# Optimization experiments

Hardware: AMD Instinct MI355X
Metric: run time of the kernel (lower is better)

## Reference

```python
import jax, jax.numpy as jnp
import numpy as np

NUM_HEADS = 4
D_MODEL = 192
NEG_INF = -1000000000.0  # fp32 branch of the original mask fill


def setup_inputs() -> dict:
    key = jax.random.key(0)
    ks = jax.random.split(key, 9)
    b, s, d = 4, 2048, D_MODEL
    inp = {
        "query": jax.random.normal(ks[0], (b, s, d), dtype=jnp.float32),
        "key": jax.random.normal(ks[1], (b, s, d), dtype=jnp.float32),
        "value": jax.random.normal(ks[2], (b, s, d), dtype=jnp.float32),
        "attn_mask": jax.random.randint(ks[3], (b, s, s), 0, 2, dtype=jnp.int32),
        "bias": jax.random.normal(ks[4], (1, NUM_HEADS, s, s), dtype=jnp.float32) * 0.1,
        # nn.Linear(d, d, bias=False) weights, applied as x @ W.T
        "Wq": jax.random.normal(ks[5], (d, d), dtype=jnp.float32) / np.sqrt(d),
        "Wk": jax.random.normal(ks[6], (d, d), dtype=jnp.float32) / np.sqrt(d),
        "Wv": jax.random.normal(ks[7], (d, d), dtype=jnp.float32) / np.sqrt(d),
        "Wo": jax.random.normal(ks[8], (d, d), dtype=jnp.float32) / np.sqrt(d),
    }
    return inp


def reference(query, key, value, attn_mask, bias, Wq, Wk, Wv, Wo):
    b, s, d = query.shape
    h, dh = NUM_HEADS, d // NUM_HEADS
    # QKV projections (Linear, no bias): x @ W.T
    q = (query @ Wq.T).reshape(b, s, h, dh)   # [b,s,h,dh]
    k = (key @ Wk.T).reshape(b, s, h, dh)
    v = (value @ Wv.T).reshape(b, s, h, dh)
    # unscaled dot-product logits (original has no 1/sqrt(d) scaling)
    logits = jnp.einsum("bqhd,bkhd->bhqk", q, k)
    logits = logits + bias                       # bias added BEFORE mask fill
    mask4 = attn_mask[:, None, :, :]             # [b,1,q,k] -> broadcast over heads
    logits = jnp.where(mask4 == 0, NEG_INF, logits)
    weights = jax.nn.softmax(logits, axis=-1)    # [b,h,q,k]
    # dropout_rate=0.0 (eval-mode / identity dropout)
    out = jnp.einsum("bhqk,bkhd->bqhd", weights, v).reshape(b, s, d)
    out = out @ Wo.T
    return out, weights.mean(axis=1)             # ([b,s,d], [b,s,s])
```

## Files before the change

### kernel.cpp

```cpp
#include <hip/hip_runtime.h>

#define BB 4
#define SS 2048
#define HH 4
#define DD 192
#define QT 16
#define NT (SS / 2 / 64)
#define NEG_BIG (-1e9f)
#define MB_NEG 0xCE6Eu

typedef __attribute__((ext_vector_type(8))) short short8;
typedef __attribute__((ext_vector_type(4))) float f32x4;

__device__ inline ushort f2bf(float x) {
    union { float f; unsigned u; } v; v.f = x;
    unsigned r = (v.u + 0x7FFFu + ((v.u >> 16) & 1u)) >> 16;
    return (ushort)r;
}
__device__ inline float bf2f(ushort x) {
    union { unsigned u; float f; } v; v.u = ((unsigned)x) << 16;
    return v.f;
}
__device__ inline void wave_lds_fence() {
    __builtin_amdgcn_wave_barrier();
    __builtin_amdgcn_s_waitcnt(0xC07F);
    __builtin_amdgcn_wave_barrier();
}

__global__ __launch_bounds__(256) void wt_kernel(
    const float* __restrict__ Wq, const float* __restrict__ Wk,
    const float* __restrict__ Wv, const float* __restrict__ Wo,
    float* __restrict__ WTall)
{
    __shared__ float tile[32][33];
    const float* W = (blockIdx.z == 0) ? Wq : (blockIdx.z == 1) ? Wk
                   : (blockIdx.z == 2) ? Wv : Wo;
    float* WT = WTall + (size_t)blockIdx.z * DD * DD;
    const int c0 = blockIdx.x * 32, j0 = blockIdx.y * 32;
    const int tx = threadIdx.x & 31, ty = threadIdx.x >> 5;
#pragma unroll
    for (int k = 0; k < 4; ++k)
        tile[ty + 8 * k][tx] = W[(size_t)(j0 + ty + 8 * k) * DD + c0 + tx];
    __syncthreads();
#pragma unroll
    for (int k = 0; k < 4; ++k)
        WT[(size_t)(c0 + ty + 8 * k) * DD + j0 + tx] = tile[tx][ty + 8 * k];
}

__global__ __launch_bounds__(192) void qkv_proj_kernel(
    const float* __restrict__ Xq, const float* __restrict__ Xk,
    const float* __restrict__ Xv, const float* __restrict__ WTall,
    ushort* __restrict__ qpad, ushort* __restrict__ kpad,
    ushort* __restrict__ vT)
{
    const int mode = blockIdx.y;
    const float* __restrict__ X = (mode == 0) ? Xq : (mode == 1) ? Xk : Xv;
    const float* __restrict__ WT = WTall + (size_t)mode * DD * DD;

    __shared__ __align__(16) float xs[16][DD];
    const int row0 = blockIdx.x * 16;
    const int t = threadIdx.x;
    {
        const float4* src = (const float4*)(X + (size_t)row0 * DD);
        float4* dst = (float4*)&xs[0][0];
        for (int i = t; i < 16 * DD / 4; i += 192) dst[i] = src[i];
    }
    __syncthreads();

    const int jt = (t % 48) * 4;
    const int rowg = t / 48;

    float acc[4][4];
#pragma unroll
    for (int r = 0; r < 4; ++r)
#pragma unroll
        for (int j = 0; j < 4; ++j) acc[r][j] = 0.f;

#pragma unroll 2
    for (int k4 = 0; k4 < DD / 4; ++k4) {
        float4 w0 = *(const float4*)&WT[(size_t)(k4 * 4 + 0) * DD + jt];
        float4 w1 = *(const float4*)&WT[(size_t)(k4 * 4 + 1) * DD + jt];
        float4 w2 = *(const float4*)&WT[(size_t)(k4 * 4 + 2) * DD + jt];
        float4 w3 = *(const float4*)&WT[(size_t)(k4 * 4 + 3) * DD + jt];
#pragma unroll
        for (int r = 0; r < 4; ++r) {
            float4 xv = *(const float4*)&xs[rowg * 4 + r][k4 * 4];
            acc[r][0] = fmaf(xv.x, w0.x, acc[r][0]); acc[r][1] = fmaf(xv.x, w0.y, acc[r][1]);
            acc[r][2] = fmaf(xv.x, w0.z, acc[r][2]); acc[r][3] = fmaf(xv.x, w0.w, acc[r][3]);
            acc[r][0] = fmaf(xv.y, w1.x, acc[r][0]); acc[r][1] = fmaf(xv.y, w1.y, acc[r][1]);
            acc[r][2] = fmaf(xv.y, w1.z, acc[r][2]); acc[r][3] = fmaf(xv.y, w1.w, acc[r][3]);
            acc[r][0] = fmaf(xv.z, w2.x, acc[r][0]); acc[r][1] = fmaf(xv.z, w2.y, acc[r][1]);
            acc[r][2] = fmaf(xv.z, w2.z, acc[r][2]); acc[r][3] = fmaf(xv.z, w2.w, acc[r][3]);
            acc[r][0] = fmaf(xv.w, w3.x, acc[r][0]); acc[r][1] = fmaf(xv.w, w3.y, acc[r][1]);
            acc[r][2] = fmaf(xv.w, w3.z, acc[r][2]); acc[r][3] = fmaf(xv.w, w3.w, acc[r][3]);
        }
    }

    if (mode < 2) {
        ushort* __restrict__ out = (mode == 0) ? qpad : kpad;
        const int hd = jt / 48, f = jt % 48;
#pragma unroll
        for (int r = 0; r < 4; ++r) {
            ushort4 o;
            o.x = f2bf(acc[r][0]); o.y = f2bf(acc[r][1]);
            o.z = f2bf(acc[r][2]); o.w = f2bf(acc[r][3]);
            *(ushort4*)&out[((size_t)(row0 + rowg * 4 + r) * HH + hd) * 64 + f] = o;
        }
        const int4 z = make_int4(0, 0, 0, 0);
        for (int i = t; i < 128; i += 192) {
            const int row = i >> 3, hh = (i >> 1) & 3, half = i & 1;
            *(int4*)&out[((size_t)(row0 + row) * HH + hh) * 64 + 48 + half * 8] = z;
        }
    } else {
        const int b = row0 >> 11, s0 = row0 & (SS - 1);
#pragma unroll
        for (int j = 0; j < 4; ++j) {
            const int col = jt + j, hd = col / 48, f = col % 48;
#pragma unroll
            for (int p = 0; p < 2; ++p) {
                unsigned pk = (unsigned)f2bf(acc[2 * p][j]) |
                              ((unsigned)f2bf(acc[2 * p + 1][j]) << 16);
                *(unsigned*)&vT[(((size_t)b * HH + hd) * 48 + f) * SS +
                                s0 + rowg * 4 + 2 * p] = pk;
            }
        }
    }
}

__device__ inline f32x4 qk_tile(const ushort* kp, short8 qa0, short8 qa1) {
    short8 kb0 = *(const short8*)(kp);
    short8 kb1 = *(const short8*)(kp + 32);
    f32x4 d = {0.f, 0.f, 0.f, 0.f};
    d = __builtin_amdgcn_mfma_f32_16x16x32_bf16(qa0, kb0, d, 0, 0, 0);
    d = __builtin_amdgcn_mfma_f32_16x16x32_bf16(qa1, kb1, d, 0, 0, 0);
    return d;
}

__global__ __launch_bounds__(512, 4) void attn_kernel(
    const ushort* __restrict__ qpad, const ushort* __restrict__ kpad,
    const ushort* __restrict__ vT, const int* __restrict__ mask,
    const float* __restrict__ bias,
    ushort* __restrict__ wscr, float* __restrict__ linv_g,
    float* __restrict__ oattn)
{
    __shared__ __align__(16) ushort wb[2][8][QT][72];
    __shared__ float l_scr[8][QT];

    const int b  = blockIdx.x >> 7;
    const int q0 = (blockIdx.x & 127) * QT;
    const int t = threadIdx.x;
    const int w = t >> 6;
    const int h = w & 3;
    const int kh = w >> 2;
    const int lane = t & 63;
    const int n16 = lane & 15, quad = lane >> 4;
    const int kbase0 = kh * (SS / 2);

    const ushort* qbase =
        qpad + ((size_t)(b * SS + q0 + n16) * HH + h) * 64 + quad * 8;
    const short8 qa0 = *(const short8*)(qbase);
    const short8 qa1 = *(const short8*)(qbase + 32);
    const ushort* kbase = kpad + (size_t)b * SS * HH * 64 + h * 64 + quad * 8;

    const int srow = lane >> 4;
    const int skey = (lane & 15) * 4;
    const int* mrow0 = mask + (size_t)(b * SS + q0) * SS + kbase0 + skey;
    const float* brow0 = bias + (size_t)(h * SS + q0) * SS + kbase0 + skey;

    float l_[4] = {0.f, 0.f, 0.f, 0.f};
    f32x4 pv[3];
#pragma unroll
    for (int nb = 0; nb < 3; ++nb) pv[nb] = (f32x4){0.f, 0.f, 0.f, 0.f};

    int4  mzc[4];
    float4 bvc[4];
#pragma unroll
    for (int rr = 0; rr < 4; ++rr) {
        const int row = rr * 4 + srow;
        mzc[rr] = *(const int4*)(mrow0 + (size_t)row * SS);
        bvc[rr] = *(const float4*)(brow0 + (size_t)row * SS);
    }
#pragma unroll
    for (int rr = 0; rr < 4; ++rr) {
        const int row = rr * 4 + srow;
        ushort4 o;
        o.x = mzc[rr].x ? f2bf(bvc[rr].x) : (ushort)MB_NEG;
        o.y = mzc[rr].y ? f2bf(bvc[rr].y) : (ushort)MB_NEG;
        o.z = mzc[rr].z ? f2bf(bvc[rr].z) : (ushort)MB_NEG;
        o.w = mzc[rr].w ? f2bf(bvc[rr].w) : (ushort)MB_NEG;
        *(ushort4*)&wb[0][w][row][skey] = o;
    }
#pragma unroll
    for (int rr = 0; rr < 4; ++rr) {
        const int row = rr * 4 + srow;
        mzc[rr] = *(const int4*)(mrow0 + (size_t)row * SS + 64);
        bvc[rr] = *(const float4*)(brow0 + (size_t)row * SS + 64);
    }
    wave_lds_fence();

    int buf = 0;
    for (int kt = 0; kt < NT; ++kt) {
        const int kb = kt * 64;

#pragma unroll
        for (int g = 0; g < 4; ++g) {
            const int key = kbase0 + kb + g * 16 + n16;
            f32x4 d = qk_tile(kbase + (size_t)key * (HH * 64), qa0, qa1);
#pragma unroll
            for (int r = 0; r < 4; ++r) {
                float wgt = __expf(d[r] + bf2f(wb[buf][w][quad * 4 + r][g * 16 + n16]));
                l_[r] += wgt;
                wb[buf][w][quad * 4 + r][g * 16 + n16] = f2bf(wgt);
            }
        }

        wave_lds_fence();

        if (kt + 1 < NT) {
#pragma unroll
            for (int rr = 0; rr < 4; ++rr) {
                const int row = rr * 4 + srow;
                ushort4 o;
                o.x = mzc[rr].x ? f2bf(bvc[rr].x) : (ushort)MB_NEG;
                o.y = mzc[rr].y ? f2bf(bvc[rr].y) : (ushort)MB_NEG;
                o.z = mzc[rr].z ? f2bf(bvc[rr].z) : (ushort)MB_NEG;
                o.w = mzc[rr].w ? f2bf(bvc[rr].w) : (ushort)MB_NEG;
                *(ushort4*)&wb[buf ^ 1][w][row][skey] = o;
            }
        }
        if (kt + 2 < NT) {
#pragma unroll
            for (int rr = 0; rr < 4; ++rr) {
                const int row = rr * 4 + srow;
                mzc[rr] = *(const int4*)(mrow0 + (size_t)row * SS + kb + 128);
                bvc[rr] = *(const float4*)(brow0 + (size_t)row * SS + kb + 128);
            }
        }

        const short8 wa0 = *(const short8*)&wb[buf][w][n16][quad * 8];
        const short8 wa1 = *(const short8*)&wb[buf][w][n16][32 + quad * 8];
#pragma unroll
        for (int nb = 0; nb < 3; ++nb) {
            const ushort* vb = vT + ((size_t)(b * HH + h) * 48 + nb * 16 + n16) * SS
                               + kbase0 + kb + quad * 8;
            short8 v0 = *(const short8*)(vb);
            short8 v1 = *(const short8*)(vb + 32);
            pv[nb] = __builtin_amdgcn_mfma_f32_16x16x32_bf16(wa0, v0, pv[nb], 0, 0, 0);
            pv[nb] = __builtin_amdgcn_mfma_f32_16x16x32_bf16(wa1, v1, pv[nb], 0, 0, 0);
        }

        {
            const int r4 = lane >> 4;
            const int k4 = (lane & 15) * 4;
#pragma unroll
            for (int it = 0; it < 4; ++it) {
                const int row = it * 4 + r4;
                ushort4 wv = *(const ushort4*)&wb[buf][w][row][k4];
                *(ushort4*)&wscr[((size_t)(b * SS + q0 + row) * HH + h) * SS +
                                 kbase0 + kb + k4] = wv;
            }
        }

        wave_lds_fence();
        buf ^= 1;
    }

#pragma unroll
    for (int r = 0; r < 4; ++r) {
        float ll = l_[r];
#pragma unroll
        for (int off = 1; off < 16; off <<= 1) ll += __shfl_xor(ll, off);
        l_[r] = ll;
    }
    if (n16 == 0) {
#pragma unroll
        for (int r = 0; r < 4; ++r) l_scr[w][quad * 4 + r] = l_[r];
    }

    __syncthreads();

    float* scr = (float*)&wb[0][0][0][0];
    if (kh == 1) {
#pragma unroll
        for (int nb = 0; nb < 3; ++nb)
            *(f32x4*)&scr[((size_t)(h * 64 + lane)) * 12 + nb * 4] = pv[nb];
    }
    __syncthreads();

    if (kh == 0) {
        float linv[4];
#pragma unroll
        for (int r = 0; r < 4; ++r)
            linv[r] = 1.0f / (l_scr[h][quad * 4 + r] + l_scr[h + 4][quad * 4 + r]);
        if (n16 == 0) {
#pragma unroll
            for (int r = 0; r < 4; ++r)
                linv_g[((size_t)b * HH + h) * SS + q0 + quad * 4 + r] = linv[r];
        }
#pragma unroll
        for (int nb = 0; nb < 3; ++nb) {
            f32x4 po = *(const f32x4*)&scr[((size_t)(h * 64 + lane)) * 12 + nb * 4];
#pragma unroll
            for (int r = 0; r < 4; ++r)
                oattn[((size_t)(b * SS + q0 + quad * 4 + r)) * DD +
                      h * 48 + nb * 16 + n16] = (pv[nb][r] + po[r]) * linv[r];
        }
    }
}

__global__ __launch_bounds__(256) void tail_kernel(
    const float* __restrict__ X,
    const float* __restrict__ WT,
    float* __restrict__ Y,
    const ushort* __restrict__ wscr, const float* __restrict__ linv_g,
    float* __restrict__ out1)
{
    __shared__ __align__(16) float xs[16][DD];
    const int t = threadIdx.x;

    if (blockIdx.x < 512) {
        const int row0 = blockIdx.x * 16;
        {
            const float4* src = (const float4*)(X + (size_t)row0 * DD);
            float4* dst = (float4*)&xs[0][0];
            for (int i = t; i < 16 * DD / 4; i += 256) dst[i] = src[i];
        }
        __syncthreads();
        if (t < 192) {
            const int jt = (t % 48) * 4;
            const int rowg = t / 48;

            float acc[4][4];
#pragma unroll
            for (int r = 0; r < 4; ++r)
#pragma unroll
                for (int j = 0; j < 4; ++j) acc[r][j] = 0.f;

#pragma unroll 2
            for (int k4 = 0; k4 < DD / 4; ++k4) {
                float4 w0 = *(const float4*)&WT[(size_t)(k4 * 4 + 0) * DD + jt];
                float4 w1 = *(const float4*)&WT[(size_t)(k4 * 4 + 1) * DD + jt];
                float4 w2 = *(const float4*)&WT[(size_t)(k4 * 4 + 2) * DD + jt];
                float4 w3 = *(const float4*)&WT[(size_t)(k4 * 4 + 3) * DD + jt];
#pragma unroll
                for (int r = 0; r < 4; ++r) {
                    float4 xv = *(const float4*)&xs[rowg * 4 + r][k4 * 4];
                    acc[r][0] = fmaf(xv.x, w0.x, acc[r][0]); acc[r][1] = fmaf(xv.x, w0.y, acc[r][1]);
                    acc[r][2] = fmaf(xv.x, w0.z, acc[r][2]); acc[r][3] = fmaf(xv.x, w0.w, acc[r][3]);
                    acc[r][0] = fmaf(xv.y, w1.x, acc[r][0]); acc[r][1] = fmaf(xv.y, w1.y, acc[r][1]);
                    acc[r][2] = fmaf(xv.y, w1.z, acc[r][2]); acc[r][3] = fmaf(xv.y, w1.w, acc[r][3]);
                    acc[r][0] = fmaf(xv.z, w2.x, acc[r][0]); acc[r][1] = fmaf(xv.z, w2.y, acc[r][1]);
                    acc[r][2] = fmaf(xv.z, w2.z, acc[r][2]); acc[r][3] = fmaf(xv.z, w2.w, acc[r][3]);
                    acc[r][0] = fmaf(xv.w, w3.x, acc[r][0]); acc[r][1] = fmaf(xv.w, w3.y, acc[r][1]);
                    acc[r][2] = fmaf(xv.w, w3.z, acc[r][2]); acc[r][3] = fmaf(xv.w, w3.w, acc[r][3]);
                }
            }

#pragma unroll
            for (int r = 0; r < 4; ++r)
                *(float4*)&Y[(size_t)(row0 + rowg * 4 + r) * DD + jt] =
                    make_float4(acc[r][0], acc[r][1], acc[r][2], acc[r][3]);
        }
    } else {
        const int bq = blockIdx.x - 512;
        const int b = bq >> 11;
        const int q = bq & (SS - 1);
        const ushort* base = wscr + (size_t)bq * (HH * SS) + t * 8;

        float li[HH];
#pragma unroll
        for (int hh = 0; hh < HH; ++hh)
            li[hh] = linv_g[((size_t)b * HH + hh) * SS + q] * 0.25f;

        float acc[8];
#pragma unroll
        for (int j = 0; j < 8; ++j) acc[j] = 0.f;

#pragma unroll
        for (int hh = 0; hh < HH; ++hh) {
            short8 wv = *(const short8*)(base + (size_t)hh * SS);
#pragma unroll
            for (int j = 0; j < 8; ++j)
                acc[j] = fmaf(bf2f((ushort)wv[j]), li[hh], acc[j]);
        }

        float* dst = out1 + (size_t)bq * SS + t * 8;
        *(float4*)dst = make_float4(acc[0], acc[1], acc[2], acc[3]);
        *(float4*)(dst + 4) = make_float4(acc[4], acc[5], acc[6], acc[7]);
    }
}

extern "C" void kernel_launch(void* const* d_in, const int* in_sizes, int n_in,
                              void* d_out, int out_size, void* d_ws, size_t ws_size,
                              hipStream_t stream)
{
    const float* query = (const float*)d_in[0];
    const float* key   = (const float*)d_in[1];
    const float* value = (const float*)d_in[2];
    const int*   amask = (const int*)d_in[3];
    const float* bias  = (const float*)d_in[4];
    const float* Wq    = (const float*)d_in[5];
    const float* Wk    = (const float*)d_in[6];
    const float* Wv    = (const float*)d_in[7];
    const float* Wo    = (const float*)d_in[8];

    const size_t n_rows = (size_t)BB * SS;
    float* out0 = (float*)d_out;
    float* out1 = out0 + n_rows * DD;

    ushort* qpad  = (ushort*)d_ws;
    ushort* kpad  = qpad + n_rows * HH * 64;
    ushort* vT    = kpad + n_rows * HH * 64;
    float*  oattn = (float*)(vT + (size_t)BB * HH * 48 * SS);
    float*  WTall = oattn + n_rows * DD;
    float*  linvg = WTall + 4 * DD * DD;
    ushort* wscr  = (ushort*)(linvg + (size_t)BB * HH * SS);

    wt_kernel<<<dim3(6, 6, 4), 256, 0, stream>>>(Wq, Wk, Wv, Wo, WTall);

    qkv_proj_kernel<<<dim3(n_rows / 16, 3), 192, 0, stream>>>(
        query, key, value, WTall, qpad, kpad, vT);

    attn_kernel<<<dim3(BB * SS / QT), 512, 0, stream>>>(
        qpad, kpad, vT, amask, bias, wscr, linvg, oattn);

    tail_kernel<<<dim3(512 + BB * SS), 256, 0, stream>>>(
        oattn, WTall + 3 * DD * DD, out0, wscr, linvg, out1);
}
```

Baseline: 378.6 us.

## Store K and V in MFMA-fragment-tiled layout for contiguous per-wave loads

The projection kernel now writes K and V into pre-swizzled 1024-element tiles that match the MFMA B-operand fragment order. Each lane in the attention kernel then reads its short8 at lane*8 within a tile, so a wave's K and V loads become fully contiguous instead of strided across rows of 256 or 2048 elements. In exchange, the projection kernel's stores are more scattered, and the index math must match the fragment mapping exactly.

```diff
diff --git a/kernel.cpp b/kernel.cpp
--- a/kernel.cpp
+++ b/kernel.cpp
@@ -50,8 +50,8 @@
 __global__ __launch_bounds__(192) void qkv_proj_kernel(
     const float* __restrict__ Xq, const float* __restrict__ Xk,
     const float* __restrict__ Xv, const float* __restrict__ WTall,
-    ushort* __restrict__ qpad, ushort* __restrict__ kpad,
-    ushort* __restrict__ vT)
+    ushort* __restrict__ qpad, ushort* __restrict__ kpadT,
+    ushort* __restrict__ vTf)
 {
     const int mode = blockIdx.y;
     const float* __restrict__ X = (mode == 0) ? Xq : (mode == 1) ? Xk : Xv;
@@ -96,49 +96,66 @@
         }
     }
 
-    if (mode < 2) {
-        ushort* __restrict__ out = (mode == 0) ? qpad : kpad;
+    const int b = row0 >> 11, s_base = row0 & (SS - 1);
+
+    if (mode == 0) {
         const int hd = jt / 48, f = jt % 48;
 #pragma unroll
         for (int r = 0; r < 4; ++r) {
             ushort4 o;
             o.x = f2bf(acc[r][0]); o.y = f2bf(acc[r][1]);
             o.z = f2bf(acc[r][2]); o.w = f2bf(acc[r][3]);
-            *(ushort4*)&out[((size_t)(row0 + rowg * 4 + r) * HH + hd) * 64 + f] = o;
+            *(ushort4*)&qpad[((size_t)(row0 + rowg * 4 + r) * HH + hd) * 64 + f] = o;
         }
         const int4 z = make_int4(0, 0, 0, 0);
         for (int i = t; i < 128; i += 192) {
             const int row = i >> 3, hh = (i >> 1) & 3, half = i & 1;
-            *(int4*)&out[((size_t)(row0 + row) * HH + hh) * 64 + 48 + half * 8] = z;
+            *(int4*)&qpad[((size_t)(row0 + row) * HH + hh) * 64 + 48 + half * 8] = z;
+        }
+    } else if (mode == 1) {
+        const int hd = jt / 48, f0 = jt % 48;
+        const int off_base = (f0 < 32)
+            ? ((f0 >> 3) * 16) * 8 + (f0 & 7)
+            : 512 + (((f0 - 32) >> 3) * 16) * 8 + (f0 & 7);
+#pragma unroll
+        for (int r = 0; r < 4; ++r) {
+            const int s = s_base + rowg * 4 + r;
+            ushort4 o;
+            o.x = f2bf(acc[r][0]); o.y = f2bf(acc[r][1]);
+            o.z = f2bf(acc[r][2]); o.w = f2bf(acc[r][3]);
+            const size_t base = ((size_t)(b * HH + hd) * (SS / 16) + (s >> 4)) * 1024;
+            *(ushort4*)&kpadT[base + off_base + (size_t)(s & 15) * 8] = o;
+        }
+        const int4 z = make_int4(0, 0, 0, 0);
+        for (int i = t; i < 128; i += 192) {
+            const int row = i >> 3, hh = (i >> 1) & 3, half = i & 1;
+            const int s = s_base + row;
+            const size_t base = ((size_t)(b * HH + hh) * (SS / 16) + (s >> 4)) * 1024;
+            *(int4*)&kpadT[base + 512 + ((size_t)((2 + half) * 16 + (s & 15))) * 8] = z;
         }
     } else {
-        const int b = row0 >> 11, s0 = row0 & (SS - 1);
 #pragma unroll
         for (int j = 0; j < 4; ++j) {
             const int col = jt + j, hd = col / 48, f = col % 48;
+            const int nb = f >> 4, dfrac = f & 15;
 #pragma unroll
             for (int p = 0; p < 2; ++p) {
+                const int s = s_base + rowg * 4 + 2 * p;
                 unsigned pk = (unsigned)f2bf(acc[2 * p][j]) |
                               ((unsigned)f2bf(acc[2 * p + 1][j]) << 16);
-                *(unsigned*)&vT[(((size_t)b * HH + hd) * 48 + f) * SS +
-                                s0 + rowg * 4 + 2 * p] = pk;
-            }
-        }
-    }
-}
-
-__device__ inline f32x4 qk_tile(const ushort* kp, short8 qa0, short8 qa1) {
-    short8 kb0 = *(const short8*)(kp);
-    short8 kb1 = *(const short8*)(kp + 32);
-    f32x4 d = {0.f, 0.f, 0.f, 0.f};
-    d = __builtin_amdgcn_mfma_f32_16x16x32_bf16(qa0, kb0, d, 0, 0, 0);
-    d = __builtin_amdgcn_mfma_f32_16x16x32_bf16(qa1, kb1, d, 0, 0, 0);
-    return d;
+                const size_t base =
+                    (((size_t)(b * HH + hd) * (SS / 64) + (s >> 6)) * 3 + nb) * 1024;
+                const int off = ((s & 63) >> 5) * 512 +
+                                (((s & 31) >> 3) * 16 + dfrac) * 8 + (s & 7);
+                *(unsigned*)&vTf[base + off] = pk;
+            }
+        }
+    }
 }
 
 __global__ __launch_bounds__(512, 4) void attn_kernel(
-    const ushort* __restrict__ qpad, const ushort* __restrict__ kpad,
-    const ushort* __restrict__ vT, const int* __restrict__ mask,
+    const ushort* __restrict__ qpad, const ushort* __restrict__ kpadT,
+    const ushort* __restrict__ vTf, const int* __restrict__ mask,
     const float* __restrict__ bias,
     ushort* __restrict__ wscr, float* __restrict__ linv_g,
     float* __restrict__ oattn)
@@ -160,7 +177,11 @@
         qpad + ((size_t)(b * SS + q0 + n16) * HH + h) * 64 + quad * 8;
     const short8 qa0 = *(const short8*)(qbase);
     const short8 qa1 = *(const short8*)(qbase + 32);
-    const ushort* kbase = kpad + (size_t)b * SS * HH * 64 + h * 64 + quad * 8;
+
+    const ushort* kT = kpadT +
+        ((size_t)(b * HH + h) * (SS / 16) + (kbase0 >> 4)) * 1024 + (size_t)lane * 8;
+    const ushort* vTb = vTf +
+        ((size_t)(b * HH + h) * (SS / 64) + (kbase0 >> 6)) * 3 * 1024 + (size_t)lane * 8;
 
     const int srow = lane >> 4;
     const int skey = (lane & 15) * 4;
@@ -204,8 +225,12 @@
 
 #pragma unroll
         for (int g = 0; g < 4; ++g) {
-            const int key = kbase0 + kb + g * 16 + n16;
-            f32x4 d = qk_tile(kbase + (size_t)key * (HH * 64), qa0, qa1);
+            const ushort* kp = kT + (size_t)(kt * 4 + g) * 1024;
+            short8 kf0 = *(const short8*)(kp);
+            short8 kf1 = *(const short8*)(kp + 512);
+            f32x4 d = {0.f, 0.f, 0.f, 0.f};
+            d = __builtin_amdgcn_mfma_f32_16x16x32_bf16(qa0, kf0, d, 0, 0, 0);
+            d = __builtin_amdgcn_mfma_f32_16x16x32_bf16(qa1, kf1, d, 0, 0, 0);
 #pragma unroll
             for (int r = 0; r < 4; ++r) {
                 float wgt = __expf(d[r] + bf2f(wb[buf][w][quad * 4 + r][g * 16 + n16]));
@@ -241,10 +266,9 @@
         const short8 wa1 = *(const short8*)&wb[buf][w][n16][32 + quad * 8];
 #pragma unroll
         for (int nb = 0; nb < 3; ++nb) {
-            const ushort* vb = vT + ((size_t)(b * HH + h) * 48 + nb * 16 + n16) * SS
-                               + kbase0 + kb + quad * 8;
-            short8 v0 = *(const short8*)(vb);
-            short8 v1 = *(const short8*)(vb + 32);
+            const ushort* vp = vTb + (size_t)(kt * 3 + nb) * 1024;
+            short8 v0 = *(const short8*)(vp);
+            short8 v1 = *(const short8*)(vp + 512);
             pv[nb] = __builtin_amdgcn_mfma_f32_16x16x32_bf16(wa0, v0, pv[nb], 0, 0, 0);
             pv[nb] = __builtin_amdgcn_mfma_f32_16x16x32_bf16(wa1, v1, pv[nb], 0, 0, 0);
         }
@@ -409,9 +433,9 @@
     float* out1 = out0 + n_rows * DD;
 
     ushort* qpad  = (ushort*)d_ws;
-    ushort* kpad  = qpad + n_rows * HH * 64;
-    ushort* vT    = kpad + n_rows * HH * 64;
-    float*  oattn = (float*)(vT + (size_t)BB * HH * 48 * SS);
+    ushort* kpadT = qpad + n_rows * HH * 64;
+    ushort* vTf   = kpadT + n_rows * HH * 64;
+    float*  oattn = (float*)(vTf + (size_t)BB * HH * 48 * SS);
     float*  WTall = oattn + n_rows * DD;
     float*  linvg = WTall + 4 * DD * DD;
     ushort* wscr  = (ushort*)(linvg + (size_t)BB * HH * SS);
@@ -419,10 +443,10 @@
     wt_kernel<<<dim3(6, 6, 4), 256, 0, stream>>>(Wq, Wk, Wv, Wo, WTall);
 
     qkv_proj_kernel<<<dim3(n_rows / 16, 3), 192, 0, stream>>>(
-        query, key, value, WTall, qpad, kpad, vT);
+        query, key, value, WTall, qpad, kpadT, vTf);
 
     attn_kernel<<<dim3(BB * SS / QT), 512, 0, stream>>>(
-        qpad, kpad, vT, amask, bias, wscr, linvg, oattn);
+        qpad, kpadT, vTf, amask, bias, wscr, linvg, oattn);
 
     tail_kernel<<<dim3(512 + BB * SS), 256, 0, stream>>>(
         oattn, WTall + 3 * DD * DD, out0, wscr, linvg, out1);
```

After: 347.9 us. 1.09x faster.
